# Kernel tuning notes

Hardware: AMD Instinct MI355X
Metric: run time of the kernel (lower is better)

Reference implementation:

```python
import jax, jax.numpy as jnp
import numpy as np

EMB = 1024
HEADS = 16
HD = EMB // HEADS

def setup_inputs() -> dict:
    key = jax.random.key(0)
    ks = jax.random.split(key, 9)
    s = 1.0 / np.sqrt(EMB)
    x = jax.random.normal(ks[0], (4, 2048, EMB), dtype=jnp.float32)
    Wq = jax.random.uniform(ks[1], (EMB, EMB), jnp.float32, -s, s)
    bq = jax.random.uniform(ks[2], (EMB,), jnp.float32, -s, s)
    Wk = jax.random.uniform(ks[3], (EMB, EMB), jnp.float32, -s, s)
    bk = jax.random.uniform(ks[4], (EMB,), jnp.float32, -s, s)
    Wv = jax.random.uniform(ks[5], (EMB, EMB), jnp.float32, -s, s)
    bv = jax.random.uniform(ks[6], (EMB,), jnp.float32, -s, s)
    Wo = jax.random.uniform(ks[7], (EMB, EMB), jnp.float32, -s, s)
    bo = jax.random.uniform(ks[8], (EMB,), jnp.float32, -s, s)
    return {"x": x, "Wq": Wq, "bq": bq, "Wk": Wk, "bk": bk, "Wv": Wv, "bv": bv, "Wo": Wo, "bo": bo}

def reference(x, Wq, bq, Wk, bk, Wv, bv, Wo, bo):
    B, T, C = x.shape
    # projections (torch Linear: y = x @ W^T + b)
    q = (x @ Wq.T + bq).reshape(B, T, HEADS, HD).transpose(0, 2, 1, 3)  # [B,H,T,hd]
    k = (x @ Wk.T + bk).reshape(B, T, HEADS, HD).transpose(0, 2, 1, 3)
    v = (x @ Wv.T + bv).reshape(B, T, HEADS, HD).transpose(0, 2, 1, 3)
    scores = jnp.einsum('bhqd,bhkd->bhqk', q, k) / jnp.sqrt(jnp.float32(HD))
    weights = jax.nn.softmax(scores, axis=-1)
    attn = jnp.einsum('bhqk,bhkd->bhqd', weights, v)
    out = attn.transpose(0, 2, 1, 3).reshape(B, T, C)
    return out @ Wo.T + bo
```

## Files before the change

kernel.cpp:

```cpp
#include <hip/hip_runtime.h>

#define TSEQ  2048
#define BATCH 4
#define NHEAD 16
#define EMB   1024

typedef __attribute__((ext_vector_type(8))) __bf16 bf16x8;
typedef __attribute__((ext_vector_type(4))) __bf16 bf16x4;
typedef __attribute__((ext_vector_type(4))) float  floatx4;
typedef __attribute__((ext_vector_type(2))) unsigned int uint32x2;
typedef __attribute__((ext_vector_type(4))) unsigned int uint32x4;

__device__ __forceinline__ void gload_lds16(const __bf16* g, __bf16* lds_uniform_base) {
  __builtin_amdgcn_global_load_lds(
      (__attribute__((address_space(1))) void*)(g),
      (__attribute__((address_space(3))) void*)(lds_uniform_base),
      16, 0, 0);
}

__global__ __launch_bounds__(256) void cvt_f32_bf16(
    const float* __restrict__ src, __bf16* __restrict__ dst)
{
  const int gid = (blockIdx.x * 256 + threadIdx.x) * 4;
  const float4 v = *(const float4*)(src + gid);
  dst[gid + 0] = (__bf16)v.x;
  dst[gid + 1] = (__bf16)v.y;
  dst[gid + 2] = (__bf16)v.z;
  dst[gid + 3] = (__bf16)v.w;
}

__global__ __launch_bounds__(256) void cvt_w4(
    const float* __restrict__ s0, const float* __restrict__ s1,
    const float* __restrict__ s2, const float* __restrict__ s3,
    __bf16* __restrict__ d0, __bf16* __restrict__ d1,
    __bf16* __restrict__ d2, __bf16* __restrict__ d3)
{
  const int z = blockIdx.z;
  const float* src = (z == 0) ? s0 : (z == 1) ? s1 : (z == 2) ? s2 : s3;
  __bf16*      dst = (z == 0) ? d0 : (z == 1) ? d1 : (z == 2) ? d2 : d3;
  const int gid = (blockIdx.x * 256 + threadIdx.x) * 4;
  const float4 v = *(const float4*)(src + gid);
  dst[gid + 0] = (__bf16)v.x;
  dst[gid + 1] = (__bf16)v.y;
  dst[gid + 2] = (__bf16)v.z;
  dst[gid + 3] = (__bf16)v.w;
}

__global__ __launch_bounds__(256) void gemm_bt_bias(
    const __bf16* __restrict__ A,
    const __bf16* __restrict__ W0, const __bf16* __restrict__ W1, const __bf16* __restrict__ W2,
    const float* __restrict__ B0, const float* __restrict__ B1, const float* __restrict__ B2,
    __bf16* __restrict__ C0, __bf16* __restrict__ C1, __bf16* __restrict__ C2)
{
  const int z = blockIdx.z;
  const __bf16* W  = (z == 0) ? W0 : ((z == 1) ? W1 : W2);
  const float*  Bb = (z == 0) ? B0 : ((z == 1) ? B1 : B2);
  __bf16*       C  = (z == 0) ? C0 : ((z == 1) ? C1 : C2);
  const float  scl = (z == 0) ? 0.125f * 1.44269504088896340736f : 1.0f;

  const int tid  = threadIdx.x;
  const int lane = tid & 63;
  const int wid  = tid >> 6;
  const int l16  = lane & 15;
  const int quad = lane >> 4;
  const int wm   = wid & 1;
  const int wn   = wid >> 1;
  const int m0   = blockIdx.y * 128;
  const int n0   = blockIdx.x * 128;

  __shared__ alignas(16) __bf16 As[128 * 32];
  __shared__ alignas(16) __bf16 Bs[128 * 32];

  floatx4 acc[4][4];
#pragma unroll
  for (int i = 0; i < 4; i++)
#pragma unroll
    for (int j = 0; j < 4; j++) acc[i][j] = (floatx4){0.f, 0.f, 0.f, 0.f};

  const int srow = tid >> 2;
  const int sseg = tid & 3;

  for (int k0 = 0; k0 < 1024; k0 += 32) {
    __syncthreads();
#pragma unroll
    for (int is = 0; is < 2; is++) {
      const int row = is * 64 + srow;
      gload_lds16(A + (size_t)(m0 + row) * 1024 + k0 + sseg * 8,
                  &As[(is * 256 + wid * 64) * 8]);
      gload_lds16(W + (size_t)(n0 + row) * 1024 + k0 + sseg * 8,
                  &Bs[(is * 256 + wid * 64) * 8]);
    }
    __syncthreads();

    bf16x8 af[4], bfr[4];
#pragma unroll
    for (int i = 0; i < 4; i++) {
      af[i]  = *(const bf16x8*)(&As[(wm * 64 + i * 16 + l16) * 32 + quad * 8]);
      bfr[i] = *(const bf16x8*)(&Bs[(wn * 64 + i * 16 + l16) * 32 + quad * 8]);
    }
#pragma unroll
    for (int i = 0; i < 4; i++)
#pragma unroll
      for (int j = 0; j < 4; j++)
        acc[i][j] = __builtin_amdgcn_mfma_f32_16x16x32_bf16(af[i], bfr[j], acc[i][j], 0, 0, 0);
  }

  float bv[4];
#pragma unroll
  for (int j = 0; j < 4; j++) bv[j] = Bb[n0 + wn * 64 + j * 16 + l16];

#pragma unroll
  for (int i = 0; i < 4; i++) {
    const size_t mrow = (size_t)m0 + wm * 64 + i * 16 + quad * 4;
#pragma unroll
    for (int j = 0; j < 4; j++) {
      const int col = n0 + wn * 64 + j * 16 + l16;
#pragma unroll
      for (int r = 0; r < 4; r++)
        C[(mrow + r) * 1024 + col] = (__bf16)((acc[i][j][r] + bv[j]) * scl);
    }
  }
}

__global__ __launch_bounds__(256) void gemm_bt_bias_f32(
    const __bf16* __restrict__ A, const __bf16* __restrict__ W,
    const float* __restrict__ Bb, float* __restrict__ C)
{
  const int tid  = threadIdx.x;
  const int lane = tid & 63;
  const int wid  = tid >> 6;
  const int l16  = lane & 15;
  const int quad = lane >> 4;
  const int wm   = wid & 1;
  const int wn   = wid >> 1;
  const int m0   = blockIdx.y * 128;
  const int n0   = blockIdx.x * 128;

  __shared__ alignas(16) __bf16 As[128 * 32];
  __shared__ alignas(16) __bf16 Bs[128 * 32];

  floatx4 acc[4][4];
#pragma unroll
  for (int i = 0; i < 4; i++)
#pragma unroll
    for (int j = 0; j < 4; j++) acc[i][j] = (floatx4){0.f, 0.f, 0.f, 0.f};

  const int srow = tid >> 2;
  const int sseg = tid & 3;

  for (int k0 = 0; k0 < 1024; k0 += 32) {
    __syncthreads();
#pragma unroll
    for (int is = 0; is < 2; is++) {
      const int row = is * 64 + srow;
      gload_lds16(A + (size_t)(m0 + row) * 1024 + k0 + sseg * 8,
                  &As[(is * 256 + wid * 64) * 8]);
      gload_lds16(W + (size_t)(n0 + row) * 1024 + k0 + sseg * 8,
                  &Bs[(is * 256 + wid * 64) * 8]);
    }
    __syncthreads();

    bf16x8 af[4], bfr[4];
#pragma unroll
    for (int i = 0; i < 4; i++) {
      af[i]  = *(const bf16x8*)(&As[(wm * 64 + i * 16 + l16) * 32 + quad * 8]);
      bfr[i] = *(const bf16x8*)(&Bs[(wn * 64 + i * 16 + l16) * 32 + quad * 8]);
    }
#pragma unroll
    for (int i = 0; i < 4; i++)
#pragma unroll
      for (int j = 0; j < 4; j++)
        acc[i][j] = __builtin_amdgcn_mfma_f32_16x16x32_bf16(af[i], bfr[j], acc[i][j], 0, 0, 0);
  }

  float bv[4];
#pragma unroll
  for (int j = 0; j < 4; j++) bv[j] = Bb[n0 + wn * 64 + j * 16 + l16];

#pragma unroll
  for (int i = 0; i < 4; i++) {
    const size_t mrow = (size_t)m0 + wm * 64 + i * 16 + quad * 4;
#pragma unroll
    for (int j = 0; j < 4; j++) {
      const int col = n0 + wn * 64 + j * 16 + l16;
#pragma unroll
      for (int r = 0; r < 4; r++)
        C[(mrow + r) * 1024 + col] = acc[i][j][r] + bv[j];
    }
  }
}

__global__ __launch_bounds__(256) void v_transpose(
    const __bf16* __restrict__ V, __bf16* __restrict__ VT)
{
  const int t0 = blockIdx.x * 64;
  const int bh = blockIdx.y;
  const int b  = bh >> 4;
  const int h  = bh & 15;
  const int tid = threadIdx.x;

  __shared__ alignas(16) __bf16 Ls[64 * 72];

  const int row = tid >> 2, seg = tid & 3;
  const __bf16* src = V + ((size_t)(b * TSEQ + t0 + row)) * EMB + h * 64;
  *(bf16x8*)(&Ls[row * 72 + seg * 8])       = *(const bf16x8*)(src + seg * 8);
  *(bf16x8*)(&Ls[row * 72 + (seg + 4) * 8]) = *(const bf16x8*)(src + (seg + 4) * 8);
  __syncthreads();

  const int od = tid >> 2, oseg = tid & 3;
  bf16x8 o0, o1;
#pragma unroll
  for (int j = 0; j < 8; j++) o0[j] = Ls[(oseg * 16 + j) * 72 + od];
#pragma unroll
  for (int j = 0; j < 8; j++) o1[j] = Ls[(oseg * 16 + 8 + j) * 72 + od];
  __bf16* dst = VT + ((size_t)bh * 64 + od) * TSEQ + t0 + oseg * 16;
  *(bf16x8*)(dst)     = o0;
  *(bf16x8*)(dst + 8) = o1;
}

#define KVB 64
#define NT  (TSEQ / KVB)

#define FA_STEP(BUF, KT)                                                                  \
  {                                                                                       \
    if ((KT) + 1 < NT) {                                                                  \
      *(bf16x8*)(&Ks[(BUF) ^ 1][soff])  = kv;                                             \
      *(bf16x8*)(&VTs[(BUF) ^ 1][soff]) = vv;                                             \
    }                                                                                     \
    if ((KT) + 2 < NT) {                                                                  \
      kv = *(const bf16x8*)(ksrc + (size_t)((KT) + 2) * KVB * EMB);                       \
      vv = *(const bf16x8*)(vsrc + ((KT) + 2) * KVB);                                     \
    }                                                                                     \
    bf16x8 pfrag[2];                                                                      \
    __builtin_amdgcn_s_setprio(1);                                                        \
    _Pragma("unroll")                                                                     \
    for (int ks = 0; ks < 2; ks++) {                                                      \
      const bf16x8 ka0 = *(const bf16x8*)(&Ks[BUF][((2 * ks) * 16 + l16) * 72 + quad * 8]);      \
      const bf16x8 ka1 = *(const bf16x8*)(&Ks[BUF][((2 * ks) * 16 + l16) * 72 + 32 + quad * 8]); \
      const bf16x8 kb0 = *(const bf16x8*)(&Ks[BUF][((2 * ks + 1) * 16 + l16) * 72 + quad * 8]);  \
      const bf16x8 kb1 = *(const bf16x8*)(&Ks[BUF][((2 * ks + 1) * 16 + l16) * 72 + 32 + quad * 8]); \
      floatx4 ta = (floatx4){0.f, 0.f, 0.f, 0.f};                                         \
      floatx4 tb = (floatx4){0.f, 0.f, 0.f, 0.f};                                         \
      ta = __builtin_amdgcn_mfma_f32_16x16x32_bf16(ka0, qf[0], ta, 0, 0, 0);              \
      ta = __builtin_amdgcn_mfma_f32_16x16x32_bf16(ka1, qf[1], ta, 0, 0, 0);              \
      tb = __builtin_amdgcn_mfma_f32_16x16x32_bf16(kb0, qf[0], tb, 0, 0, 0);              \
      tb = __builtin_amdgcn_mfma_f32_16x16x32_bf16(kb1, qf[1], tb, 0, 0, 0);              \
      bf16x4 pa, pb;                                                                      \
      float ps = 0.f;                                                                     \
      _Pragma("unroll")                                                                   \
      for (int r = 0; r < 4; r++) {                                                       \
        const float e = __builtin_amdgcn_exp2f(ta[r]);                                    \
        ps += e; pa[r] = (__bf16)e;                                                       \
      }                                                                                   \
      _Pragma("unroll")                                                                   \
      for (int r = 0; r < 4; r++) {                                                       \
        const float e = __builtin_amdgcn_exp2f(tb[r]);                                    \
        ps += e; pb[r] = (__bf16)e;                                                       \
      }                                                                                   \
      l_r += ps;                                                                          \
      const uint32x2 A2 = __builtin_bit_cast(uint32x2, pa);                               \
      const uint32x2 B2 = __builtin_bit_cast(uint32x2, pb);                               \
      const uint32x2 r0 = __builtin_amdgcn_permlane32_swap(A2.x, B2.x, false, false);     \
      const uint32x2 r1 = __builtin_amdgcn_permlane32_swap(A2.y, B2.y, false, false);     \
      const uint32x2 s0 = __builtin_amdgcn_permlane16_swap(r0.x, r0.y, false, false);     \
      const uint32x2 s1 = __builtin_amdgcn_permlane16_swap(r1.x, r1.y, false, false);     \
      const uint32x4 fw = (uint32x4){s0.x, s1.x, s0.y, s1.y};                             \
      pfrag[ks] = __builtin_bit_cast(bf16x8, fw);                                         \
    }                                                                                     \
    _Pragma("unroll")                                                                     \
    for (int dg = 0; dg < 4; dg++) {                                                      \
      _Pragma("unroll")                                                                   \
      for (int ks = 0; ks < 2; ks++) {                                                    \
        const bf16x8 vf = *(const bf16x8*)(&VTs[BUF][(dg * 16 + l16) * 72 + ks * 32 + quad * 8]); \
        Oacc[dg] = __builtin_amdgcn_mfma_f32_16x16x32_bf16(vf, pfrag[ks], Oacc[dg], 0, 0, 0);     \
      }                                                                                   \
    }                                                                                     \
    __builtin_amdgcn_s_setprio(0);                                                        \
    __syncthreads();                                                                      \
  }

__global__ __launch_bounds__(512, 4) void flash_attn(
    const __bf16* __restrict__ Q, const __bf16* __restrict__ K,
    const __bf16* __restrict__ VT, __bf16* __restrict__ O)
{
  const int qt   = blockIdx.x;
  const int bh   = blockIdx.y;
  const int b    = bh >> 4;
  const int h    = bh & 15;
  const int tid  = threadIdx.x;
  const int wid  = tid >> 6;
  const int lane = tid & 63;
  const int l16  = lane & 15;
  const int quad = lane >> 4;

  __shared__ alignas(16) __bf16 Ks[2][KVB * 72];
  __shared__ alignas(16) __bf16 VTs[2][64 * 72];

  const size_t base = ((size_t)b * TSEQ) * EMB + (size_t)h * 64;
  const __bf16* qptr  = Q + base;
  const __bf16* kptr  = K + base;
  const __bf16* vtptr = VT + (size_t)bh * 64 * TSEQ;
  __bf16*       optr  = O + base;

  const int qb = qt * 128 + wid * 16;

  bf16x8 qf[2];
#pragma unroll
  for (int hf = 0; hf < 2; hf++)
    qf[hf] = *(const bf16x8*)(qptr + (size_t)(qb + l16) * EMB + hf * 32 + quad * 8);

  floatx4 Oacc[4];
#pragma unroll
  for (int dg = 0; dg < 4; dg++) Oacc[dg] = (floatx4){0.f, 0.f, 0.f, 0.f};
  float l_r = 0.f;

  const int srow = tid >> 3, sseg = tid & 7;
  const __bf16* ksrc = kptr  + (size_t)srow * EMB  + sseg * 8;
  const __bf16* vsrc = vtptr + (size_t)srow * TSEQ + sseg * 8;
  const int soff = srow * 72 + sseg * 8;

  bf16x8 kv = *(const bf16x8*)(ksrc);
  bf16x8 vv = *(const bf16x8*)(vsrc);
  *(bf16x8*)(&Ks[0][soff])  = kv;
  *(bf16x8*)(&VTs[0][soff]) = vv;
  kv = *(const bf16x8*)(ksrc + (size_t)KVB * EMB);
  vv = *(const bf16x8*)(vsrc + KVB);
  __syncthreads();

#pragma unroll 1
  for (int kt = 0; kt < NT; kt += 2) {
    FA_STEP(0, kt);
    FA_STEP(1, kt + 1);
  }

  float l = l_r;
  l += __shfl_xor(l, 16);
  l += __shfl_xor(l, 32);
  const float inv = 1.0f / l;
#pragma unroll
  for (int dg = 0; dg < 4; dg++) {
    bf16x4 ov;
#pragma unroll
    for (int r = 0; r < 4; r++) ov[r] = (__bf16)(Oacc[dg][r] * inv);
    *(bf16x4*)(optr + (size_t)(qb + l16) * EMB + dg * 16 + quad * 4) = ov;
  }
}

extern "C" void kernel_launch(void* const* d_in, const int* in_sizes, int n_in,
                              void* d_out, int out_size, void* d_ws, size_t ws_size,
                              hipStream_t stream) {
  const float* x  = (const float*)d_in[0];
  const float* Wq = (const float*)d_in[1];
  const float* bq = (const float*)d_in[2];
  const float* Wk = (const float*)d_in[3];
  const float* bk = (const float*)d_in[4];
  const float* Wv = (const float*)d_in[5];
  const float* bv = (const float*)d_in[6];
  const float* Wo = (const float*)d_in[7];
  const float* bo = (const float*)d_in[8];
  float* out = (float*)d_out;

  const size_t NELEM = (size_t)BATCH * TSEQ * EMB;
  const size_t WELEM = (size_t)EMB * EMB;

  __bf16* q_b  = (__bf16*)d_out;
  __bf16* k_b  = q_b + NELEM;
  __bf16* x_b  = (__bf16*)d_ws;
  __bf16* v_b  = x_b + NELEM;
  __bf16* wq_b = v_b + NELEM;
  __bf16* wk_b = wq_b + WELEM;
  __bf16* wv_b = wk_b + WELEM;
  __bf16* wo_b = wv_b + WELEM;

  dim3 blk(256, 1, 1);

  cvt_f32_bf16<<<(int)(NELEM / 1024), blk, 0, stream>>>(x, x_b);
  cvt_w4<<<dim3((int)(WELEM / 1024), 1, 4), blk, 0, stream>>>(
      Wq, Wk, Wv, Wo, wq_b, wk_b, wv_b, wo_b);

  gemm_bt_bias<<<dim3(8, 64, 3), blk, 0, stream>>>(
      x_b, wq_b, wk_b, wv_b, bq, bk, bv, q_b, k_b, v_b);

  v_transpose<<<dim3(TSEQ / 64, BATCH * NHEAD), blk, 0, stream>>>(v_b, x_b);

  flash_attn<<<dim3(TSEQ / 128, BATCH * NHEAD), dim3(512, 1, 1), 0, stream>>>(
      q_b, k_b, x_b, v_b);

  gemm_bt_bias_f32<<<dim3(8, 64, 1), blk, 0, stream>>>(v_b, wo_b, bo, out);
}
```

Before: 296.8 us.

## Process two query groups per wave in flash attention and swizzle block order

Flash attention now uses 256-thread blocks where each wave handles 32 query rows (two 16-row groups). This reuses every K/V fragment loaded from LDS across two MFMA groups. The softmax row sum is computed with an MFMA against a ones vector instead of scalar adds, and block indices are swizzled in both GEMMs and attention to improve L2 locality. In exchange it needs more registers per wave and has fewer waves per block to hide latency.

```diff
diff --git a/kernel.cpp b/kernel.cpp
--- a/kernel.cpp
+++ b/kernel.cpp
@@ -65,8 +65,10 @@
   const int quad = lane >> 4;
   const int wm   = wid & 1;
   const int wn   = wid >> 1;
-  const int m0   = blockIdx.y * 128;
-  const int n0   = blockIdx.x * 128;
+  const int lin = blockIdx.x + blockIdx.y * 8;
+  const int swz = (lin & 7) * 64 + (lin >> 3);
+  const int m0  = (swz >> 3) * 128;
+  const int n0  = (swz & 7) * 128;
 
   __shared__ alignas(16) __bf16 As[128 * 32];
   __shared__ alignas(16) __bf16 Bs[128 * 32];
@@ -133,8 +135,10 @@
   const int quad = lane >> 4;
   const int wm   = wid & 1;
   const int wn   = wid >> 1;
-  const int m0   = blockIdx.y * 128;
-  const int n0   = blockIdx.x * 128;
+  const int lin = blockIdx.x + blockIdx.y * 8;
+  const int swz = (lin & 7) * 64 + (lin >> 3);
+  const int m0  = (swz >> 3) * 128;
+  const int n0  = (swz & 7) * 128;
 
   __shared__ alignas(16) __bf16 As[128 * 32];
   __shared__ alignas(16) __bf16 Bs[128 * 32];
@@ -224,67 +228,75 @@
 #define FA_STEP(BUF, KT)                                                                  \
   {                                                                                       \
     if ((KT) + 1 < NT) {                                                                  \
-      *(bf16x8*)(&Ks[(BUF) ^ 1][soff])  = kv;                                             \
-      *(bf16x8*)(&VTs[(BUF) ^ 1][soff]) = vv;                                             \
+      *(bf16x8*)(&Ks[(BUF) ^ 1][soff])            = kv0;                                  \
+      *(bf16x8*)(&Ks[(BUF) ^ 1][soff + 32 * 72])  = kv1;                                  \
+      *(bf16x8*)(&VTs[(BUF) ^ 1][soff])           = vv0;                                  \
+      *(bf16x8*)(&VTs[(BUF) ^ 1][soff + 32 * 72]) = vv1;                                  \
     }                                                                                     \
     if ((KT) + 2 < NT) {                                                                  \
-      kv = *(const bf16x8*)(ksrc + (size_t)((KT) + 2) * KVB * EMB);                       \
-      vv = *(const bf16x8*)(vsrc + ((KT) + 2) * KVB);                                     \
+      kv0 = *(const bf16x8*)(ksrc + (size_t)(((KT) + 2) * KVB) * EMB);                    \
+      kv1 = *(const bf16x8*)(ksrc + (size_t)(((KT) + 2) * KVB + 32) * EMB);               \
+      vv0 = *(const bf16x8*)(vsrc + ((KT) + 2) * KVB);                                    \
+      vv1 = *(const bf16x8*)(vsrc + (size_t)32 * TSEQ + ((KT) + 2) * KVB);                \
     }                                                                                     \
-    bf16x8 pfrag[2];                                                                      \
     __builtin_amdgcn_s_setprio(1);                                                        \
+    bf16x8 pfrag[2][2];                                                                   \
     _Pragma("unroll")                                                                     \
     for (int ks = 0; ks < 2; ks++) {                                                      \
       const bf16x8 ka0 = *(const bf16x8*)(&Ks[BUF][((2 * ks) * 16 + l16) * 72 + quad * 8]);      \
       const bf16x8 ka1 = *(const bf16x8*)(&Ks[BUF][((2 * ks) * 16 + l16) * 72 + 32 + quad * 8]); \
       const bf16x8 kb0 = *(const bf16x8*)(&Ks[BUF][((2 * ks + 1) * 16 + l16) * 72 + quad * 8]);  \
       const bf16x8 kb1 = *(const bf16x8*)(&Ks[BUF][((2 * ks + 1) * 16 + l16) * 72 + 32 + quad * 8]); \
-      floatx4 ta = (floatx4){0.f, 0.f, 0.f, 0.f};                                         \
-      floatx4 tb = (floatx4){0.f, 0.f, 0.f, 0.f};                                         \
-      ta = __builtin_amdgcn_mfma_f32_16x16x32_bf16(ka0, qf[0], ta, 0, 0, 0);              \
-      ta = __builtin_amdgcn_mfma_f32_16x16x32_bf16(ka1, qf[1], ta, 0, 0, 0);              \
-      tb = __builtin_amdgcn_mfma_f32_16x16x32_bf16(kb0, qf[0], tb, 0, 0, 0);              \
-      tb = __builtin_amdgcn_mfma_f32_16x16x32_bf16(kb1, qf[1], tb, 0, 0, 0);              \
-      bf16x4 pa, pb;                                                                      \
-      float ps = 0.f;                                                                     \
       _Pragma("unroll")                                                                   \
-      for (int r = 0; r < 4; r++) {                                                       \
-        const float e = __builtin_amdgcn_exp2f(ta[r]);                                    \
-        ps += e; pa[r] = (__bf16)e;                                                       \
+      for (int g = 0; g < 2; g++) {                                                       \
+        floatx4 ta = (floatx4){0.f, 0.f, 0.f, 0.f};                                       \
+        floatx4 tb = (floatx4){0.f, 0.f, 0.f, 0.f};                                       \
+        ta = __builtin_amdgcn_mfma_f32_16x16x32_bf16(ka0, qf[g][0], ta, 0, 0, 0);         \
+        ta = __builtin_amdgcn_mfma_f32_16x16x32_bf16(ka1, qf[g][1], ta, 0, 0, 0);         \
+        tb = __builtin_amdgcn_mfma_f32_16x16x32_bf16(kb0, qf[g][0], tb, 0, 0, 0);         \
+        tb = __builtin_amdgcn_mfma_f32_16x16x32_bf16(kb1, qf[g][1], tb, 0, 0, 0);         \
+        bf16x4 pa, pb;                                                                    \
+        _Pragma("unroll")                                                                 \
+        for (int r = 0; r < 4; r++) pa[r] = (__bf16)__builtin_amdgcn_exp2f(ta[r]);        \
+        _Pragma("unroll")                                                                 \
+        for (int r = 0; r < 4; r++) pb[r] = (__bf16)__builtin_amdgcn_exp2f(tb[r]);        \
+        const uint32x2 A2 = __builtin_bit_cast(uint32x2, pa);                             \
+        const uint32x2 B2 = __builtin_bit_cast(uint32x2, pb);                             \
+        const uint32x2 r0 = __builtin_amdgcn_permlane32_swap(A2.x, B2.x, false, false);   \
+        const uint32x2 r1 = __builtin_amdgcn_permlane32_swap(A2.y, B2.y, false, false);   \
+        const uint32x2 s0 = __builtin_amdgcn_permlane16_swap(r0.x, r0.y, false, false);   \
+        const uint32x2 s1 = __builtin_amdgcn_permlane16_swap(r1.x, r1.y, false, false);   \
+        const uint32x4 fw = (uint32x4){s0.x, s1.x, s0.y, s1.y};                           \
+        pfrag[g][ks] = __builtin_bit_cast(bf16x8, fw);                                    \
       }                                                                                   \
-      _Pragma("unroll")                                                                   \
-      for (int r = 0; r < 4; r++) {                                                       \
-        const float e = __builtin_amdgcn_exp2f(tb[r]);                                    \
-        ps += e; pb[r] = (__bf16)e;                                                       \
-      }                                                                                   \
-      l_r += ps;                                                                          \
-      const uint32x2 A2 = __builtin_bit_cast(uint32x2, pa);                               \
-      const uint32x2 B2 = __builtin_bit_cast(uint32x2, pb);                               \
-      const uint32x2 r0 = __builtin_amdgcn_permlane32_swap(A2.x, B2.x, false, false);     \
-      const uint32x2 r1 = __builtin_amdgcn_permlane32_swap(A2.y, B2.y, false, false);     \
-      const uint32x2 s0 = __builtin_amdgcn_permlane16_swap(r0.x, r0.y, false, false);     \
-      const uint32x2 s1 = __builtin_amdgcn_permlane16_swap(r1.x, r1.y, false, false);     \
-      const uint32x4 fw = (uint32x4){s0.x, s1.x, s0.y, s1.y};                             \
-      pfrag[ks] = __builtin_bit_cast(bf16x8, fw);                                         \
+    }                                                                                     \
+    _Pragma("unroll")                                                                     \
+    for (int g = 0; g < 2; g++) {                                                         \
+      lacc[g] = __builtin_amdgcn_mfma_f32_16x16x32_bf16(ones, pfrag[g][0], lacc[g], 0, 0, 0); \
+      lacc[g] = __builtin_amdgcn_mfma_f32_16x16x32_bf16(ones, pfrag[g][1], lacc[g], 0, 0, 0); \
     }                                                                                     \
     _Pragma("unroll")                                                                     \
     for (int dg = 0; dg < 4; dg++) {                                                      \
       _Pragma("unroll")                                                                   \
       for (int ks = 0; ks < 2; ks++) {                                                    \
         const bf16x8 vf = *(const bf16x8*)(&VTs[BUF][(dg * 16 + l16) * 72 + ks * 32 + quad * 8]); \
-        Oacc[dg] = __builtin_amdgcn_mfma_f32_16x16x32_bf16(vf, pfrag[ks], Oacc[dg], 0, 0, 0);     \
+        _Pragma("unroll")                                                                 \
+        for (int g = 0; g < 2; g++)                                                       \
+          Oacc[g][dg] = __builtin_amdgcn_mfma_f32_16x16x32_bf16(vf, pfrag[g][ks], Oacc[g][dg], 0, 0, 0); \
       }                                                                                   \
     }                                                                                     \
     __builtin_amdgcn_s_setprio(0);                                                        \
     __syncthreads();                                                                      \
   }
 
-__global__ __launch_bounds__(512, 4) void flash_attn(
+__global__ __launch_bounds__(256, 4) void flash_attn(
     const __bf16* __restrict__ Q, const __bf16* __restrict__ K,
     const __bf16* __restrict__ VT, __bf16* __restrict__ O)
 {
-  const int qt   = blockIdx.x;
-  const int bh   = blockIdx.y;
+  const int lin = blockIdx.x + blockIdx.y * 16;
+  const int swz = (lin & 7) * 128 + (lin >> 3);
+  const int qt  = swz & 15;
+  const int bh  = swz >> 4;
   const int b    = bh >> 4;
   const int h    = bh & 15;
   const int tid  = threadIdx.x;
@@ -302,29 +314,44 @@
   const __bf16* vtptr = VT + (size_t)bh * 64 * TSEQ;
   __bf16*       optr  = O + base;
 
-  const int qb = qt * 128 + wid * 16;
-
-  bf16x8 qf[2];
-#pragma unroll
-  for (int hf = 0; hf < 2; hf++)
-    qf[hf] = *(const bf16x8*)(qptr + (size_t)(qb + l16) * EMB + hf * 32 + quad * 8);
-
-  floatx4 Oacc[4];
-#pragma unroll
-  for (int dg = 0; dg < 4; dg++) Oacc[dg] = (floatx4){0.f, 0.f, 0.f, 0.f};
-  float l_r = 0.f;
+  const int qb = qt * 128 + wid * 32;
+
+  bf16x8 qf[2][2];
+#pragma unroll
+  for (int g = 0; g < 2; g++)
+#pragma unroll
+    for (int hf = 0; hf < 2; hf++)
+      qf[g][hf] = *(const bf16x8*)(qptr + (size_t)(qb + g * 16 + l16) * EMB + hf * 32 + quad * 8);
+
+  floatx4 Oacc[2][4];
+#pragma unroll
+  for (int g = 0; g < 2; g++)
+#pragma unroll
+    for (int dg = 0; dg < 4; dg++) Oacc[g][dg] = (floatx4){0.f, 0.f, 0.f, 0.f};
+  floatx4 lacc[2];
+#pragma unroll
+  for (int g = 0; g < 2; g++) lacc[g] = (floatx4){0.f, 0.f, 0.f, 0.f};
+
+  const uint32x4 onesw = (uint32x4){0x3F803F80u, 0x3F803F80u, 0x3F803F80u, 0x3F803F80u};
+  const bf16x8 ones = __builtin_bit_cast(bf16x8, onesw);
 
   const int srow = tid >> 3, sseg = tid & 7;
   const __bf16* ksrc = kptr  + (size_t)srow * EMB  + sseg * 8;
   const __bf16* vsrc = vtptr + (size_t)srow * TSEQ + sseg * 8;
   const int soff = srow * 72 + sseg * 8;
 
-  bf16x8 kv = *(const bf16x8*)(ksrc);
-  bf16x8 vv = *(const bf16x8*)(vsrc);
-  *(bf16x8*)(&Ks[0][soff])  = kv;
-  *(bf16x8*)(&VTs[0][soff]) = vv;
-  kv = *(const bf16x8*)(ksrc + (size_t)KVB * EMB);
-  vv = *(const bf16x8*)(vsrc + KVB);
+  bf16x8 kv0 = *(const bf16x8*)(ksrc);
+  bf16x8 kv1 = *(const bf16x8*)(ksrc + (size_t)32 * EMB);
+  bf16x8 vv0 = *(const bf16x8*)(vsrc);
+  bf16x8 vv1 = *(const bf16x8*)(vsrc + (size_t)32 * TSEQ);
+  *(bf16x8*)(&Ks[0][soff])            = kv0;
+  *(bf16x8*)(&Ks[0][soff + 32 * 72])  = kv1;
+  *(bf16x8*)(&VTs[0][soff])           = vv0;
+  *(bf16x8*)(&VTs[0][soff + 32 * 72]) = vv1;
+  kv0 = *(const bf16x8*)(ksrc + (size_t)KVB * EMB);
+  kv1 = *(const bf16x8*)(ksrc + (size_t)(KVB + 32) * EMB);
+  vv0 = *(const bf16x8*)(vsrc + KVB);
+  vv1 = *(const bf16x8*)(vsrc + (size_t)32 * TSEQ + KVB);
   __syncthreads();
 
 #pragma unroll 1
@@ -333,16 +360,16 @@
     FA_STEP(1, kt + 1);
   }
 
-  float l = l_r;
-  l += __shfl_xor(l, 16);
-  l += __shfl_xor(l, 32);
-  const float inv = 1.0f / l;
-#pragma unroll
-  for (int dg = 0; dg < 4; dg++) {
-    bf16x4 ov;
-#pragma unroll
-    for (int r = 0; r < 4; r++) ov[r] = (__bf16)(Oacc[dg][r] * inv);
-    *(bf16x4*)(optr + (size_t)(qb + l16) * EMB + dg * 16 + quad * 4) = ov;
+#pragma unroll
+  for (int g = 0; g < 2; g++) {
+    const float inv = 1.0f / lacc[g][0];
+#pragma unroll
+    for (int dg = 0; dg < 4; dg++) {
+      bf16x4 ov;
+#pragma unroll
+      for (int r = 0; r < 4; r++) ov[r] = (__bf16)(Oacc[g][dg][r] * inv);
+      *(bf16x4*)(optr + (size_t)(qb + g * 16 + l16) * EMB + dg * 16 + quad * 4) = ov;
+    }
   }
 }
 
@@ -383,7 +410,7 @@
 
   v_transpose<<<dim3(TSEQ / 64, BATCH * NHEAD), blk, 0, stream>>>(v_b, x_b);
 
-  flash_attn<<<dim3(TSEQ / 128, BATCH * NHEAD), dim3(512, 1, 1), 0, stream>>>(
+  flash_attn<<<dim3(TSEQ / 128, BATCH * NHEAD), blk, 0, stream>>>(
       q_b, k_b, x_b, v_b);
 
   gemm_bt_bias_f32<<<dim3(8, 64, 1), blk, 0, stream>>>(v_b, wo_b, bo, out);
```

Measured after the change: 274.1 us. 7.6% less time.
